# Performance work log

Hardware: AMD Instinct MI355X
Metric: run time of the kernel (lower is better)

The kernel has to match this reference:

```python
import jax, jax.numpy as jnp
import numpy as np


def _vieta_pell_basis(x, degree):
    # Iterative recurrence: V0 = 2, V1 = x, Vn = x*V_{n-1} + V_{n-2}
    basis = [2.0 * jnp.ones_like(x), x]
    for _ in range(2, degree + 1):
        basis.append(x * basis[-1] + basis[-2])
    return jnp.stack(basis[: degree + 1], axis=-1)  # [b, i, d+1]


def setup_inputs() -> dict:
    key = jax.random.key(0)
    k1, k2 = jax.random.split(key)
    batch, input_dim, output_dim, degree = 4096, 1024, 1024, 8
    x = jax.random.normal(k1, (batch, input_dim), dtype=jnp.float32)
    std = 1.0 / (input_dim * (degree + 1))
    vp_coeffs = jax.random.normal(k2, (input_dim, output_dim, degree + 1), dtype=jnp.float32) * std
    return {"x": x, "vp_coeffs": vp_coeffs}


def reference(x, vp_coeffs):
    degree = vp_coeffs.shape[-1] - 1
    xt = jnp.tanh(x)  # [b, i]
    vp_basis = _vieta_pell_basis(xt, degree)  # [b, i, d+1]
    y = jnp.einsum("bid,iod->bo", vp_basis, vp_coeffs)
    return y
```

## Files before the change

kernel.cpp:

```cpp
#include <hip/hip_runtime.h>
#include <hip/hip_bf16.h>

typedef unsigned short u16;
typedef unsigned int   u32;
typedef unsigned long long u64;

#define BATCH 4096
#define IDIM  1024
#define ODIM  1024
#define NDEG  9
#define KTOT  (IDIM * NDEG)

#define BM 128
#define BN 128
#define BKK 64

typedef __attribute__((ext_vector_type(8))) short short8_t;
typedef __attribute__((ext_vector_type(4))) float f32x4;

__device__ __forceinline__ u16 f2bf(float f) {
    union { float f; u32 u; } v; v.f = f;
    u32 r = v.u + 0x7FFFu + ((v.u >> 16) & 1u);
    return (u16)(r >> 16);
}
__device__ __forceinline__ u32 pack2bf(float lo, float hi) {
    return (u32)f2bf(lo) | ((u32)f2bf(hi) << 16);
}

__device__ __forceinline__ void gl_lds16(const u16* g, u16* l) {
    __builtin_amdgcn_global_load_lds(
        (const __attribute__((address_space(1))) void*)g,
        (__attribute__((address_space(3))) void*)l,
        16, 0, 0);
}

__global__ void prep_a_kernel(const float* __restrict__ x, u16* __restrict__ A) {
    int t  = blockIdx.x * 256 + threadIdx.x;
    int b  = t >> 9;
    int i2 = (t & 511) << 1;
    float2 xv = ((const float2*)x)[t];
    float t0 = tanhf(xv.x), t1 = tanhf(xv.y);
    u32* dst = (u32*)(A + (size_t)b * KTOT + i2);
    float a0 = 2.0f, a1 = 2.0f;
    float b0 = t0,  b1 = t1;
    dst[0]   = pack2bf(2.0f, 2.0f);
    dst[512] = pack2bf(t0, t1);
#pragma unroll
    for (int d = 2; d < NDEG; ++d) {
        float n0 = t0 * b0 + a0;
        float n1 = t1 * b1 + a1;
        dst[(size_t)d * 512] = pack2bf(n0, n1);
        a0 = b0; b0 = n0; a1 = b1; b1 = n1;
    }
}

#define PB_TI 128
#define PB_TO 8
#define PB_J  (PB_TO * NDEG)
#define PB_LS 132

__global__ void prep_b_kernel(const float* __restrict__ c, u16* __restrict__ Bt) {
    __shared__ u16 lds[PB_J * PB_LS];
    const int tid = threadIdx.x;
    const int i0  = blockIdx.y * PB_TI;
    const int o0  = blockIdx.x * PB_TO;
    const float* src = c + (size_t)i0 * (ODIM * NDEG) + (size_t)o0 * NDEG;

#pragma unroll
    for (int t = 0; t < 36; ++t) {
        int f  = t * 256 + tid;
        int ii = f / PB_J;
        int j  = f - ii * PB_J;
        float v = src[(size_t)ii * (ODIM * NDEG) + j];
        lds[j * PB_LS + ii] = f2bf(v);
    }
    __syncthreads();

#pragma unroll
    for (int t = 0; t < 9; ++t) {
        int g   = t * 256 + tid;
        int j   = g >> 5;
        int ii4 = (g & 31) << 2;
        int o   = j / NDEG;
        int d   = j - o * NDEG;
        u64 v = *(const u64*)(lds + j * PB_LS + ii4);
        *(u64*)(Bt + (size_t)(o0 + o) * KTOT + d * 1024 + i0 + ii4) = v;
    }
}

__global__ __launch_bounds__(256, 4)
void gemm_kernel(const u16* __restrict__ A, const u16* __restrict__ B,
                 float* __restrict__ C, int kLen) {
    __shared__ __align__(16) u16 ldsA[BM * BKK];
    __shared__ __align__(16) u16 ldsB[BN * BKK];

    const int tid  = threadIdx.x;
    const int lane = tid & 63;
    const int wave = tid >> 6;
    const int quad = lane >> 4;
    const int l15  = lane & 15;
    const int wm   = wave & 1;
    const int wn   = wave >> 1;
    const int bm   = blockIdx.y;
    const int bn   = blockIdx.x;
    const int kStart = blockIdx.z * kLen;
    C += (size_t)blockIdx.z * BATCH * ODIM;

    const u16* ga[4]; const u16* gb[4];
    u16* la[4]; u16* lb[4];
#pragma unroll
    for (int t = 0; t < 4; ++t) {
        int s  = t * 256 + tid;
        int r  = s >> 3;
        int sc = (s & 7) ^ (r & 7);
        ga[t] = A + (size_t)(bm * BM + r) * KTOT + kStart + sc * 8;
        gb[t] = B + (size_t)(bn * BN + r) * KTOT + kStart + sc * 8;
        la[t] = ldsA + s * 8;
        lb[t] = ldsB + s * 8;
    }

    f32x4 acc[4][4];
#pragma unroll
    for (int mt = 0; mt < 4; ++mt)
#pragma unroll
        for (int nt = 0; nt < 4; ++nt)
            acc[mt][nt] = (f32x4){0.f, 0.f, 0.f, 0.f};

    const int nIter = kLen / BKK;
    for (int it = 0; it < nIter; ++it) {
#pragma unroll
        for (int t = 0; t < 4; ++t) gl_lds16(ga[t], la[t]);
#pragma unroll
        for (int t = 0; t < 4; ++t) gl_lds16(gb[t], lb[t]);
        __syncthreads();

#pragma unroll
        for (int kk = 0; kk < 2; ++kk) {
            short8_t af[4], bfg[4];
#pragma unroll
            for (int mt = 0; mt < 4; ++mt) {
                int row = wm * 64 + mt * 16 + l15;
                int pc  = (kk * 4 + quad) ^ (row & 7);
                af[mt] = *(const short8_t*)(ldsA + (row * 8 + pc) * 8);
            }
#pragma unroll
            for (int nt = 0; nt < 4; ++nt) {
                int row = wn * 64 + nt * 16 + l15;
                int pc  = (kk * 4 + quad) ^ (row & 7);
                bfg[nt] = *(const short8_t*)(ldsB + (row * 8 + pc) * 8);
            }
#pragma unroll
            for (int mt = 0; mt < 4; ++mt)
#pragma unroll
                for (int nt = 0; nt < 4; ++nt)
                    acc[mt][nt] = __builtin_amdgcn_mfma_f32_16x16x32_bf16(
                        af[mt], bfg[nt], acc[mt][nt], 0, 0, 0);
        }
        __syncthreads();

#pragma unroll
        for (int t = 0; t < 4; ++t) { ga[t] += BKK; gb[t] += BKK; }
    }

#pragma unroll
    for (int mt = 0; mt < 4; ++mt) {
#pragma unroll
        for (int nt = 0; nt < 4; ++nt) {
            int row0 = bm * BM + wm * 64 + mt * 16 + quad * 4;
            int col  = bn * BN + wn * 64 + nt * 16 + l15;
#pragma unroll
            for (int r = 0; r < 4; ++r)
                C[(size_t)(row0 + r) * ODIM + col] = acc[mt][nt][r];
        }
    }
}

__global__ void reduce_kernel(const float* __restrict__ P, float* __restrict__ out,
                              int S) {
    int t = blockIdx.x * 256 + threadIdx.x;
    f32x4 a = ((const f32x4*)P)[t];
    for (int s = 1; s < S; ++s)
        a += ((const f32x4*)(P + (size_t)s * BATCH * ODIM))[t];
    ((f32x4*)out)[t] = a;
}

extern "C" void kernel_launch(void* const* d_in, const int* in_sizes, int n_in,
                              void* d_out, int out_size, void* d_ws, size_t ws_size,
                              hipStream_t stream) {
    const float* x      = (const float*)d_in[0];
    const float* coeffs = (const float*)d_in[1];
    float* out = (float*)d_out;

    u16* A  = (u16*)d_ws;
    u16* Bt = A + (size_t)BATCH * KTOT;
    float* P = (float*)(Bt + (size_t)ODIM * KTOT);

    size_t need_base = ((size_t)BATCH * KTOT + (size_t)ODIM * KTOT) * 2;
    size_t per_part  = (size_t)BATCH * ODIM * 4;

    prep_a_kernel<<<BATCH * IDIM / 512, 256, 0, stream>>>(x, A);
    {
        dim3 g(ODIM / PB_TO, IDIM / PB_TI);
        prep_b_kernel<<<g, 256, 0, stream>>>(coeffs, Bt);
    }

    int S = 1;
    if (ws_size >= need_base + 4 * per_part) S = 4;
    else if (ws_size >= need_base + 2 * per_part) S = 2;

    if (S > 1) {
        dim3 grid(ODIM / BN, BATCH / BM, S);
        gemm_kernel<<<grid, 256, 0, stream>>>(A, Bt, P, KTOT / S);
        reduce_kernel<<<BATCH * ODIM / 1024, 256, 0, stream>>>(P, out, S);
    } else {
        dim3 grid(ODIM / BN, BATCH / BM, 1);
        gemm_kernel<<<grid, 256, 0, stream>>>(A, Bt, out, KTOT);
    }
}
```

Measured before the change: 220.8 us.

## Fuse prep kernels with output zeroing and replace split-K reduce with atomics

Merges the A-basis and B-transpose prep kernels into one launch that also zeroes the output buffer. The GEMM now always uses a 2-way K split and accumulates directly into the output with float atomicAdd, which removes the partial buffers and the separate reduce kernel. Launch bounds change from 4 to 2 waves per SIMD occupancy hint. This saves launches and the partial-sum write and read traffic, at the cost of atomic contention and a result whose summation order is not fixed.

```diff
diff --git a/kernel.cpp b/kernel.cpp
--- a/kernel.cpp
+++ b/kernel.cpp
@@ -34,61 +34,74 @@
         16, 0, 0);
 }
 
-__global__ void prep_a_kernel(const float* __restrict__ x, u16* __restrict__ A) {
-    int t  = blockIdx.x * 256 + threadIdx.x;
-    int b  = t >> 9;
-    int i2 = (t & 511) << 1;
-    float2 xv = ((const float2*)x)[t];
-    float t0 = tanhf(xv.x), t1 = tanhf(xv.y);
-    u32* dst = (u32*)(A + (size_t)b * KTOT + i2);
-    float a0 = 2.0f, a1 = 2.0f;
-    float b0 = t0,  b1 = t1;
-    dst[0]   = pack2bf(2.0f, 2.0f);
-    dst[512] = pack2bf(t0, t1);
-#pragma unroll
-    for (int d = 2; d < NDEG; ++d) {
-        float n0 = t0 * b0 + a0;
-        float n1 = t1 * b1 + a1;
-        dst[(size_t)d * 512] = pack2bf(n0, n1);
-        a0 = b0; b0 = n0; a1 = b1; b1 = n1;
-    }
-}
-
 #define PB_TI 128
 #define PB_TO 8
 #define PB_J  (PB_TO * NDEG)
 #define PB_LS 132
 
-__global__ void prep_b_kernel(const float* __restrict__ c, u16* __restrict__ Bt) {
+#define NB_B   1024
+#define NB_A   8192
+#define NB_Z   256
+
+__global__ void prep_kernel(const float* __restrict__ x,
+                            const float* __restrict__ c,
+                            u16* __restrict__ A, u16* __restrict__ Bt,
+                            float* __restrict__ out) {
     __shared__ u16 lds[PB_J * PB_LS];
+    const int bb  = blockIdx.x;
     const int tid = threadIdx.x;
-    const int i0  = blockIdx.y * PB_TI;
-    const int o0  = blockIdx.x * PB_TO;
-    const float* src = c + (size_t)i0 * (ODIM * NDEG) + (size_t)o0 * NDEG;
-
-#pragma unroll
-    for (int t = 0; t < 36; ++t) {
-        int f  = t * 256 + tid;
-        int ii = f / PB_J;
-        int j  = f - ii * PB_J;
-        float v = src[(size_t)ii * (ODIM * NDEG) + j];
-        lds[j * PB_LS + ii] = f2bf(v);
-    }
-    __syncthreads();
-
-#pragma unroll
-    for (int t = 0; t < 9; ++t) {
-        int g   = t * 256 + tid;
-        int j   = g >> 5;
-        int ii4 = (g & 31) << 2;
-        int o   = j / NDEG;
-        int d   = j - o * NDEG;
-        u64 v = *(const u64*)(lds + j * PB_LS + ii4);
-        *(u64*)(Bt + (size_t)(o0 + o) * KTOT + d * 1024 + i0 + ii4) = v;
-    }
-}
-
-__global__ __launch_bounds__(256, 4)
+
+    if (bb < NB_B) {
+        const int i0 = (bb & 7) * PB_TI;
+        const int o0 = (bb >> 3) * PB_TO;
+        const float* src = c + (size_t)i0 * (ODIM * NDEG) + (size_t)o0 * NDEG;
+#pragma unroll
+        for (int t = 0; t < 36; ++t) {
+            int f  = t * 256 + tid;
+            int ii = f / PB_J;
+            int j  = f - ii * PB_J;
+            float v = src[(size_t)ii * (ODIM * NDEG) + j];
+            lds[j * PB_LS + ii] = f2bf(v);
+        }
+        __syncthreads();
+#pragma unroll
+        for (int t = 0; t < 9; ++t) {
+            int g   = t * 256 + tid;
+            int j   = g >> 5;
+            int ii4 = (g & 31) << 2;
+            int o   = j / NDEG;
+            int d   = j - o * NDEG;
+            u64 v = *(const u64*)(lds + j * PB_LS + ii4);
+            *(u64*)(Bt + (size_t)(o0 + o) * KTOT + d * 1024 + i0 + ii4) = v;
+        }
+    } else if (bb < NB_B + NB_A) {
+        int t  = (bb - NB_B) * 256 + tid;
+        int b  = t >> 9;
+        int i2 = (t & 511) << 1;
+        float2 xv = ((const float2*)x)[t];
+        float t0 = tanhf(xv.x), t1 = tanhf(xv.y);
+        u32* dst = (u32*)(A + (size_t)b * KTOT + i2);
+        float a0 = 2.0f, a1 = 2.0f;
+        float b0 = t0,  b1 = t1;
+        dst[0]   = pack2bf(2.0f, 2.0f);
+        dst[512] = pack2bf(t0, t1);
+#pragma unroll
+        for (int d = 2; d < NDEG; ++d) {
+            float n0 = t0 * b0 + a0;
+            float n1 = t1 * b1 + a1;
+            dst[(size_t)d * 512] = pack2bf(n0, n1);
+            a0 = b0; b0 = n0; a1 = b1; b1 = n1;
+        }
+    } else {
+        int t = (bb - NB_B - NB_A) * 256 + tid;
+        f32x4 z = (f32x4){0.f, 0.f, 0.f, 0.f};
+#pragma unroll
+        for (int r = 0; r < 16; ++r)
+            ((f32x4*)out)[(size_t)r * (NB_Z * 256) + t] = z;
+    }
+}
+
+__global__ __launch_bounds__(256, 2)
 void gemm_kernel(const u16* __restrict__ A, const u16* __restrict__ B,
                  float* __restrict__ C, int kLen) {
     __shared__ __align__(16) u16 ldsA[BM * BKK];
@@ -104,7 +117,6 @@
     const int bm   = blockIdx.y;
     const int bn   = blockIdx.x;
     const int kStart = blockIdx.z * kLen;
-    C += (size_t)blockIdx.z * BATCH * ODIM;
 
     const u16* ga[4]; const u16* gb[4];
     u16* la[4]; u16* lb[4];
@@ -170,18 +182,9 @@
             int col  = bn * BN + wn * 64 + nt * 16 + l15;
 #pragma unroll
             for (int r = 0; r < 4; ++r)
-                C[(size_t)(row0 + r) * ODIM + col] = acc[mt][nt][r];
-        }
-    }
-}
-
-__global__ void reduce_kernel(const float* __restrict__ P, float* __restrict__ out,
-                              int S) {
-    int t = blockIdx.x * 256 + threadIdx.x;
-    f32x4 a = ((const f32x4*)P)[t];
-    for (int s = 1; s < S; ++s)
-        a += ((const f32x4*)(P + (size_t)s * BATCH * ODIM))[t];
-    ((f32x4*)out)[t] = a;
+                atomicAdd(&C[(size_t)(row0 + r) * ODIM + col], acc[mt][nt][r]);
+        }
+    }
 }
 
 extern "C" void kernel_launch(void* const* d_in, const int* in_sizes, int n_in,
@@ -193,27 +196,9 @@
 
     u16* A  = (u16*)d_ws;
     u16* Bt = A + (size_t)BATCH * KTOT;
-    float* P = (float*)(Bt + (size_t)ODIM * KTOT);
-
-    size_t need_base = ((size_t)BATCH * KTOT + (size_t)ODIM * KTOT) * 2;
-    size_t per_part  = (size_t)BATCH * ODIM * 4;
-
-    prep_a_kernel<<<BATCH * IDIM / 512, 256, 0, stream>>>(x, A);
-    {
-        dim3 g(ODIM / PB_TO, IDIM / PB_TI);
-        prep_b_kernel<<<g, 256, 0, stream>>>(coeffs, Bt);
-    }
-
-    int S = 1;
-    if (ws_size >= need_base + 4 * per_part) S = 4;
-    else if (ws_size >= need_base + 2 * per_part) S = 2;
-
-    if (S > 1) {
-        dim3 grid(ODIM / BN, BATCH / BM, S);
-        gemm_kernel<<<grid, 256, 0, stream>>>(A, Bt, P, KTOT / S);
-        reduce_kernel<<<BATCH * ODIM / 1024, 256, 0, stream>>>(P, out, S);
-    } else {
-        dim3 grid(ODIM / BN, BATCH / BM, 1);
-        gemm_kernel<<<grid, 256, 0, stream>>>(A, Bt, out, KTOT);
-    }
-}
+
+    prep_kernel<<<NB_B + NB_A + NB_Z, 256, 0, stream>>>(x, coeffs, A, Bt, out);
+
+    dim3 grid(ODIM / BN, BATCH / BM, 2);
+    gemm_kernel<<<grid, 256, 0, stream>>>(A, Bt, out, KTOT / 2);
+}
```

Result: faster. 216.4 us (-2.0%).
